# Optimization experiments

Measured on AMD Instinct MI355X. Metric: run time of the kernel, lower is better.

The kernel has to match this reference:

```python
import jax, jax.numpy as jnp
import numpy as np

WAY, NQ, C, FS = 5, 4096, 64, 5
T = FS * FS            # 25 spatial tokens
EMB = T + 1            # feature_size**2 + feature_proj_dim = 26
HEADS = 2
HD = EMB // HEADS      # 13
SCALE = HD ** -0.5
T_ATTN = 5.0           # args.temperature_attn
TEMP = 0.2             # args.temperature
LN_EPS = 1e-6


def _ln(x, g, b):
    m = x.mean(-1, keepdims=True)
    v = jnp.mean((x - m) ** 2, axis=-1, keepdims=True)
    return (x - m) / jnp.sqrt(v + LN_EPS) * g + b


def _block(x, p):
    # pre-LN transformer block (timm-style), x: (B, T, EMB)
    h = _ln(x, p['ln1_g'], p['ln1_b'])
    qkv = h @ p['qkv_w'].T + p['qkv_b']                       # (B,T,3*EMB)
    B, N, _ = qkv.shape
    qkv = qkv.reshape(B, N, 3, HEADS, HD).transpose(2, 0, 3, 1, 4)
    q, k, v = qkv[0], qkv[1], qkv[2]                          # (B,H,T,hd)
    a = jax.nn.softmax(jnp.einsum('bhqd,bhkd->bhqk', q, k) * SCALE, axis=-1)
    o = jnp.einsum('bhqk,bhkd->bhqd', a, v).transpose(0, 2, 1, 3).reshape(B, N, EMB)
    x = x + o @ p['attn_w'].T + p['attn_b']
    h = _ln(x, p['ln2_g'], p['ln2_b'])
    h = jax.nn.gelu(h @ p['fc1_w'].T + p['fc1_b'], approximate=False)
    return x + h @ p['fc2_w'].T + p['fc2_b']


def _decoder(corr, src, tgt, p):
    # CATs TransformerAggregator, num_hyperpixel=1, depth=1
    # corr: (B,1,T,T); src/tgt: (B,1,T,1) projected features
    pos = jnp.concatenate([
        jnp.broadcast_to(p['pos_x'], (1, 1, FS, FS, EMB // 2)),
        jnp.broadcast_to(p['pos_y'], (1, 1, FS, FS, EMB // 2))], axis=-1).reshape(1, 1, T, EMB)
    B = corr.shape[0]
    x = jnp.concatenate([jnp.swapaxes(corr, -1, -2), tgt], axis=3) + pos
    x = _block(x.reshape(B, T, EMB), p)
    x = (x @ p['dec_w'].T + p['dec_b']).reshape(B, 1, T, T)
    x = jnp.swapaxes(x, -1, -2) + corr            # swap axes for second self-attn pass
    x = jnp.concatenate([x, src], axis=3) + pos
    x = _block(x.reshape(B, T, EMB), p)           # same block weights reused
    x = (x @ p['dec_w'].T + p['dec_b']).reshape(B, 1, T, T) + corr
    return x.mean(axis=1)                         # (B,T,T)


def _forward(spt, qry, proj_w, proj_b, pos_x, pos_y, ln1_g, ln1_b, qkv_w, qkv_b,
             attn_w, attn_b, ln2_g, ln2_b, fc1_w, fc1_b, fc2_w, fc2_b, dec_w, dec_b):
    p = dict(pos_x=pos_x, pos_y=pos_y, ln1_g=ln1_g, ln1_b=ln1_b, qkv_w=qkv_w,
             qkv_b=qkv_b, attn_w=attn_w, attn_b=attn_b, ln2_g=ln2_g, ln2_b=ln2_b,
             fc1_w=fc1_w, fc1_b=fc1_b, fc2_w=fc2_w, fc2_b=fc2_b, dec_w=dec_w, dec_b=dec_b)
    # normalize_feature: subtract channel mean
    spt = spt - spt.mean(axis=1, keepdims=True)
    qry = qry - qry.mean(axis=1, keepdims=True)
    spt_f = jnp.broadcast_to(spt[None], (NQ, WAY, C, FS, FS)).reshape(-1, C, FS, FS)
    qry_f = jnp.broadcast_to(qry[:, None], (NQ, WAY, C, FS, FS)).reshape(-1, C, FS, FS)

    def l2n(x):  # FeatureL2Norm over channel dim
        return x / jnp.sqrt(jnp.sum(x * x, axis=1, keepdims=True) + 1e-6)

    s = l2n(spt_f).reshape(-1, C, T)
    t = l2n(qry_f).reshape(-1, C, T)
    corr = jnp.einsum('bci,bcj->bij', s, t)[:, None]                  # (B,1,T,T)
    sp = (jnp.swapaxes(spt_f.reshape(-1, C, T), 1, 2) @ proj_w.T + proj_b)[:, None]
    tp = (jnp.swapaxes(qry_f.reshape(-1, C, T), 1, 2) @ proj_w.T + proj_b)[:, None]
    refined = _decoder(corr, sp, tp, p)                               # (B,T,T)

    corr_s = refined.reshape(NQ, WAY, T, FS, FS)
    corr_q = refined.reshape(NQ, WAY, FS, FS, T)

    def gnorm(x, axis):  # torch.var is unbiased (ddof=1)
        m = x.mean(axis=axis, keepdims=True)
        v = jnp.var(x, axis=axis, keepdims=True, ddof=1)
        return (x - m) / jnp.sqrt(v + 1e-5)

    corr_s = jax.nn.softmax(gnorm(corr_s, 2) / T_ATTN, axis=2).reshape(NQ, WAY, FS, FS, FS, FS)
    corr_q = jax.nn.softmax(gnorm(corr_q, 4) / T_ATTN, axis=4).reshape(NQ, WAY, FS, FS, FS, FS)
    attn_s = corr_s.sum(axis=(4, 5))                                  # (NQ,WAY,FS,FS)
    attn_q = corr_q.sum(axis=(2, 3))
    spt_att = attn_s[:, :, None] * spt[None]                          # (NQ,WAY,C,FS,FS)
    qry_att = attn_q[:, :, None] * qry[:, None]
    sp_p = spt_att.mean(axis=(-1, -2))                                # (NQ,WAY,C)
    qp_p = qry_att.mean(axis=(-1, -2))
    n1 = jnp.maximum(jnp.linalg.norm(sp_p, axis=-1), 1e-8)
    n2 = jnp.maximum(jnp.linalg.norm(qp_p, axis=-1), 1e-8)
    sim = jnp.sum(sp_p * qp_p, axis=-1) / (n1 * n2)                   # (NQ,WAY)
    return sim / TEMP


def setup_inputs() -> dict:
    key = jax.random.key(0)
    ks = jax.random.split(key, 12)

    def w(i, shape, s=0.02):
        return jax.random.normal(ks[i], shape, jnp.float32) * s

    return {
        'spt': jax.random.normal(ks[0], (WAY, C, FS, FS), jnp.float32),
        'qry': jax.random.normal(ks[1], (NQ, C, FS, FS), jnp.float32),
        'proj_w': w(2, (1, C)), 'proj_b': jnp.zeros((1,), jnp.float32),
        'pos_x': w(3, (1, 1, 1, FS, EMB // 2)),
        'pos_y': w(4, (1, 1, FS, 1, EMB // 2)),
        'ln1_g': jnp.ones((EMB,), jnp.float32), 'ln1_b': jnp.zeros((EMB,), jnp.float32),
        'qkv_w': w(5, (3 * EMB, EMB)), 'qkv_b': jnp.zeros((3 * EMB,), jnp.float32),
        'attn_w': w(6, (EMB, EMB)), 'attn_b': jnp.zeros((EMB,), jnp.float32),
        'ln2_g': jnp.ones((EMB,), jnp.float32), 'ln2_b': jnp.zeros((EMB,), jnp.float32),
        'fc1_w': w(7, (4 * EMB, EMB)), 'fc1_b': jnp.zeros((4 * EMB,), jnp.float32),
        'fc2_w': w(8, (EMB, 4 * EMB)), 'fc2_b': jnp.zeros((EMB,), jnp.float32),
        'dec_w': w(9, (T, EMB)), 'dec_b': jnp.zeros((T,), jnp.float32),
    }


def reference(spt, qry, proj_w, proj_b, pos_x, pos_y, ln1_g, ln1_b, qkv_w, qkv_b,
              attn_w, attn_b, ln2_g, ln2_b, fc1_w, fc1_b, fc2_w, fc2_b, dec_w, dec_b):
    return _forward(spt, qry, proj_w, proj_b, pos_x, pos_y, ln1_g, ln1_b, qkv_w, qkv_b,
                    attn_w, attn_b, ln2_g, ln2_b, fc1_w, fc1_b, fc2_w, fc2_b, dec_w, dec_b)
```

## Files before the change

### kernel.cpp

```cpp
#include <hip/hip_runtime.h>
#include <math.h>

#define WAYS 5
#define NQN 4096
#define NBATCH (NQN*WAYS)

#define WS_SC 0
#define WS_RS 8000
#define WS_SP 8125
#define WS_QM 8250
#define WS_QR 110650
#define WS_TP 213050

#define WSYNC() do { asm volatile("s_waitcnt lgkmcnt(0)" ::: "memory"); __builtin_amdgcn_wave_barrier(); } while(0)

__global__ void prep_spt(const float* __restrict__ spt, const float* __restrict__ proj_w,
                         const float* __restrict__ proj_b, float* __restrict__ ws) {
    int tid = threadIdx.x;
    if (tid >= 125) return;
    int w = tid / 25, i = tid % 25;
    const float* base = spt + w * 1600 + i;
    float s = 0.f;
    for (int c = 0; c < 64; c++) s += base[c * 25];
    float m = s * (1.f / 64.f);
    float ss = 0.f, pj = 0.f;
    for (int c = 0; c < 64; c++) {
        float v = base[c * 25] - m;
        ss += v * v; pj += v * proj_w[c];
    }
    float rinv = rsqrtf(ss + 1e-6f);
    for (int c = 0; c < 64; c++)
        ws[WS_SC + (w * 25 + i) * 64 + c] = (base[c * 25] - m) * rinv;
    ws[WS_RS + w * 25 + i] = rinv;
    ws[WS_SP + w * 25 + i] = pj + proj_b[0];
}

__global__ void prep_qry(const float* __restrict__ qry, const float* __restrict__ proj_w,
                         const float* __restrict__ proj_b, float* __restrict__ ws) {
    int idx = blockIdx.x * 256 + threadIdx.x;
    if (idx >= NQN * 25) return;
    int q = idx / 25, j = idx % 25;
    const float* base = qry + q * 1600 + j;
    float s = 0.f;
    for (int c = 0; c < 64; c++) s += base[c * 25];
    float m = s * (1.f / 64.f);
    float ss = 0.f, pj = 0.f;
    for (int c = 0; c < 64; c++) {
        float v = base[c * 25] - m;
        ss += v * v; pj += v * proj_w[c];
    }
    ws[WS_QM + idx] = m;
    ws[WS_QR + idx] = rsqrtf(ss + 1e-6f);
    ws[WS_TP + idx] = pj + proj_b[0];
}

template<int M, int N, int K, int TM, int TN, int SA, int WN, int SO, int VW,
         bool ADD, bool GELU>
__device__ __forceinline__ void mmw(const float* __restrict__ A, const float* __restrict__ W,
                                    const float* __restrict__ bias, float* __restrict__ O,
                                    int lane) {
    static_assert(M % TM == 0 && N % TN == 0, "tile");
    static_assert(K % VW == 0, "vec");
    constexpr int GM = M / TM, GN = N / TN, ITEMS = GM * GN;
    constexpr int FULL = (ITEMS / 64) * 64;
    constexpr int REMO = (ITEMS - FULL) * TM * TN;
    constexpr bool SCT = (ITEMS > FULL) && (REMO <= 64);
    constexpr int LIM = SCT ? FULL : ITEMS;

    for (int v = lane; v < LIM; v += 64) {
        const int m0 = (v / GN) * TM, n0 = (v % GN) * TN;
        float acc[TM][TN];
#pragma unroll
        for (int a = 0; a < TM; a++)
#pragma unroll
            for (int c = 0; c < TN; c++) acc[a][c] = 0.f;

        if constexpr (VW == 4) {
#pragma unroll
            for (int k = 0; k < K; k += 4) {
                float4 av[TM], wv[TN];
#pragma unroll
                for (int a = 0; a < TM; a++) av[a] = *(const float4*)(A + (m0 + a) * SA + k);
#pragma unroll
                for (int c = 0; c < TN; c++) wv[c] = *(const float4*)(W + (n0 + c) * WN + k);
#pragma unroll
                for (int a = 0; a < TM; a++)
#pragma unroll
                    for (int c = 0; c < TN; c++) {
                        acc[a][c] += av[a].x * wv[c].x;
                        acc[a][c] += av[a].y * wv[c].y;
                        acc[a][c] += av[a].z * wv[c].z;
                        acc[a][c] += av[a].w * wv[c].w;
                    }
            }
        } else {
#pragma unroll 4
            for (int k = 0; k < K; k += 2) {
                float2 av[TM], wv[TN];
#pragma unroll
                for (int a = 0; a < TM; a++) av[a] = *(const float2*)(A + (m0 + a) * SA + k);
#pragma unroll
                for (int c = 0; c < TN; c++) wv[c] = *(const float2*)(W + (n0 + c) * WN + k);
#pragma unroll
                for (int a = 0; a < TM; a++)
#pragma unroll
                    for (int c = 0; c < TN; c++) {
                        acc[a][c] += av[a].x * wv[c].x;
                        acc[a][c] += av[a].y * wv[c].y;
                    }
            }
        }
#pragma unroll
        for (int a = 0; a < TM; a++)
#pragma unroll
            for (int c = 0; c < TN; c++) {
                int n = n0 + c;
                float r = acc[a][c] + (bias ? bias[n] : 0.f);
                if (GELU) r = 0.5f * r * (1.f + erff(r * 0.70710678118654752f));
                if (ADD) O[(m0 + a) * SO + n] += r; else O[(m0 + a) * SO + n] = r;
            }
    }
    if constexpr (SCT) {
        if (lane < REMO) {
            const int t = FULL + lane / (TM * TN), r0 = lane % (TM * TN);
            const int m = (t / GN) * TM + r0 / TN, n = (t % GN) * TN + r0 % TN;
            float acc = 0.f;
#pragma unroll 4
            for (int k = 0; k < K; k += 2) {
                float2 a2 = *(const float2*)(A + m * SA + k);
                float2 w2 = *(const float2*)(W + n * WN + k);
                acc += a2.x * w2.x;
                acc += a2.y * w2.y;
            }
            float r = acc + (bias ? bias[n] : 0.f);
            if (GELU) r = 0.5f * r * (1.f + erff(r * 0.70710678118654752f));
            if (ADD) O[m * SO + n] += r; else O[m * SO + n] = r;
        }
    }
}

__device__ __forceinline__ void ln_row(const float* __restrict__ x, float* __restrict__ h,
                                       const float* __restrict__ g, const float* __restrict__ bb) {
    float s = 0.f;
#pragma unroll
    for (int e = 0; e < 26; e++) s += x[e];
    float m = s * (1.f / 26.f);
    float vv = 0.f;
#pragma unroll
    for (int e = 0; e < 26; e++) { float d = x[e] - m; vv += d * d; }
    float r = rsqrtf(vv * (1.f / 26.f) + 1e-6f);
#pragma unroll
    for (int e = 0; e < 26; e++) h[e] = (x[e] - m) * r * g[e] + bb[e];
}

__global__ void __launch_bounds__(256, 2)
fused_kernel(const float* __restrict__ qry, const float* __restrict__ ws,
             const float* __restrict__ pos_x, const float* __restrict__ pos_y,
             const float* __restrict__ qkv_w, const float* __restrict__ qkv_b,
             const float* __restrict__ attn_w, const float* __restrict__ attn_b,
             const float* __restrict__ ln1_g, const float* __restrict__ ln1_b,
             const float* __restrict__ ln2_g, const float* __restrict__ ln2_b,
             const float* __restrict__ fc1_w, const float* __restrict__ fc1_b,
             const float* __restrict__ fc2_w, const float* __restrict__ fc2_b,
             const float* __restrict__ dec_w, const float* __restrict__ dec_b,
             float* __restrict__ out) {
    __shared__ __align__(16) float lds[4][4096];
    const int wid = threadIdx.x >> 6, lane = threadIdx.x & 63;
    const int b = blockIdx.x * 4 + wid, q = b / WAYS, w = b % WAYS;

    float* xm    = lds[wid];
    float* hm    = xm + 650;
    float* corrm = xm + 1300;
    float* sm    = xm + 1925;
    float* scr   = xm + 1992;

    if (lane < 25) {
        sm[lane]      = ws[WS_QM + q * 25 + lane];
        sm[32 + lane] = ws[WS_QR + q * 25 + lane];
    }
    WSYNC();

    for (int e = lane; e < 1600; e += 64) {
        int c = e / 25, j = e - c * 25;
        scr[j * 68 + c] = (qry[q * 1600 + e] - sm[j]) * sm[32 + j];
    }
    WSYNC();

    mmw<25, 25, 64, 5, 1, 64, 68, 25, 4, false, false>(ws + WS_SC + w * 1600, scr, nullptr, corrm, lane);
    WSYNC();

    for (int e = lane; e < 650; e += 64) {
        int t = e / 26, d = e - t * 26;
        float p = (d < 13) ? pos_x[(t % 5) * 13 + d] : pos_y[(t / 5) * 13 + (d - 13)];
        float base = (d < 25) ? corrm[d * 25 + t] : ws[WS_TP + q * 25 + t];
        xm[e] = base + p;
    }
    WSYNC();

    for (int it = 0; it < 2; ++it) {
        if (lane < 25) ln_row(xm + lane * 26, hm + lane * 26, ln1_g, ln1_b);
        WSYNC();
        mmw<25, 26, 26, 5, 2, 26, 26, 84, 2, false, false>(hm, qkv_w,        qkv_b,      scr,      lane);
        mmw<25, 26, 26, 5, 2, 26, 26, 84, 2, false, false>(hm, qkv_w + 676,  qkv_b + 26, scr + 28, lane);
        mmw<25, 26, 26, 5, 2, 26, 26, 84, 2, false, false>(hm, qkv_w + 1352, qkv_b + 52, scr + 56, lane);
        WSYNC();
        if (lane < 50) {
            int h = lane / 25, i = lane - h * 25;
            const float* qb = scr + i * 84 + h * 13;
            float qv[13];
#pragma unroll
            for (int k = 0; k < 13; k++) qv[k] = qb[k];
            float P[25];
            float mx = -1e30f;
#pragma unroll
            for (int j = 0; j < 25; j++) {
                const float* kb = scr + j * 84 + 28 + h * 13;
                float a = 0.f;
#pragma unroll
                for (int k = 0; k < 13; k++) a += qv[k] * kb[k];
                a *= 0.27735009811261457f;
                P[j] = a; mx = fmaxf(mx, a);
            }
            float s = 0.f;
#pragma unroll
            for (int j = 0; j < 25; j++) { P[j] = __expf(P[j] - mx); s += P[j]; }
            float inv = 1.f / s;
            float o[13];
#pragma unroll
            for (int n = 0; n < 13; n++) o[n] = 0.f;
#pragma unroll
            for (int k = 0; k < 25; k++) {
                const float* vb = scr + k * 84 + 56 + h * 13;
                float p = P[k];
#pragma unroll
                for (int n = 0; n < 13; n++) o[n] += p * vb[n];
            }
            float* ob = hm + i * 26 + h * 13;
#pragma unroll
            for (int n = 0; n < 13; n++) ob[n] = o[n] * inv;
        }
        WSYNC();
        mmw<25, 26, 26, 5, 2, 26, 26, 26, 2, true, false>(hm, attn_w, attn_b, xm, lane);
        WSYNC();
        if (lane < 25) ln_row(xm + lane * 26, hm + lane * 26, ln2_g, ln2_b);
        WSYNC();
        mmw<25, 52, 26, 5, 4, 26, 26, 52, 2, false, true>(hm, fc1_w, fc1_b, scr, lane);
        WSYNC();
        mmw<25, 26, 52, 5, 2, 52, 104, 26, 2, true, false>(scr, fc2_w, fc2_b, xm, lane);
        WSYNC();
        mmw<25, 52, 26, 5, 4, 26, 26, 52, 2, false, true>(hm, fc1_w + 1352, fc1_b + 52, scr, lane);
        WSYNC();
        mmw<25, 26, 52, 5, 2, 52, 104, 26, 2, true, false>(scr, fc2_w + 52, nullptr, xm, lane);
        WSYNC();
        mmw<25, 25, 26, 5, 1, 26, 26, 25, 2, false, false>(xm, dec_w, dec_b, scr, lane);
        WSYNC();
        if (it == 0) {
            for (int e = lane; e < 650; e += 64) {
                int t = e / 26, d = e - t * 26;
                float p = (d < 13) ? pos_x[(t % 5) * 13 + d] : pos_y[(t / 5) * 13 + (d - 13)];
                float base = (d < 25) ? (scr[d * 25 + t] + corrm[t * 25 + d]) : ws[WS_SP + w * 25 + t];
                xm[e] = base + p;
            }
            WSYNC();
        }
    }

    for (int e = lane; e < 625; e += 64) scr[e] += corrm[e];
    WSYNC();

    if (lane < 25) {
        int j = lane;
        float s = 0.f;
        for (int i = 0; i < 25; i++) s += scr[i * 25 + j];
        float m = s * 0.04f;
        float ss = 0.f;
        for (int i = 0; i < 25; i++) { float d = scr[i * 25 + j] - m; ss += d * d; }
        float rinv = rsqrtf(ss * (1.f / 24.f) + 1e-5f) * 0.2f;
        float mx = -1e30f;
        for (int i = 0; i < 25; i++) { float z = (scr[i * 25 + j] - m) * rinv; corrm[i * 25 + j] = z; mx = fmaxf(mx, z); }
        float se = 0.f;
        for (int i = 0; i < 25; i++) { float e2 = __expf(corrm[i * 25 + j] - mx); corrm[i * 25 + j] = e2; se += e2; }
        float inv = 1.f / se;
        for (int i = 0; i < 25; i++) corrm[i * 25 + j] *= inv;
    }
    WSYNC();
    if (lane < 25) {
        int i = lane; float s = 0.f;
        for (int j = 0; j < 25; j++) s += corrm[i * 25 + j];
        hm[i] = s * 0.04f / ws[WS_RS + w * 25 + i];
    }
    WSYNC();
    if (lane < 25) {
        int i = lane;
        float s = 0.f;
        for (int j = 0; j < 25; j++) s += scr[i * 25 + j];
        float m = s * 0.04f;
        float ss = 0.f;
        for (int j = 0; j < 25; j++) { float d = scr[i * 25 + j] - m; ss += d * d; }
        float rinv = rsqrtf(ss * (1.f / 24.f) + 1e-5f) * 0.2f;
        float mx = -1e30f;
        for (int j = 0; j < 25; j++) { float z = (scr[i * 25 + j] - m) * rinv; corrm[i * 25 + j] = z; mx = fmaxf(mx, z); }
        float se = 0.f;
        for (int j = 0; j < 25; j++) { float e2 = __expf(corrm[i * 25 + j] - mx); corrm[i * 25 + j] = e2; se += e2; }
        float inv = 1.f / se;
        for (int j = 0; j < 25; j++) corrm[i * 25 + j] *= inv;
    }
    WSYNC();
    if (lane < 25) {
        int j = lane; float s = 0.f;
        for (int i = 0; i < 25; i++) s += corrm[i * 25 + j];
        hm[32 + j] = s * 0.04f / sm[32 + j];
    }
    WSYNC();

    for (int e = lane; e < 1600; e += 64) {
        int c = e / 25, j = e - c * 25;
        scr[e] = (qry[q * 1600 + e] - sm[j]) * sm[32 + j];
    }
    WSYNC();

    {
        float sv = 0.f, qv2 = 0.f;
        const float* snb = ws + WS_SC + w * 1600 + lane;
        for (int i = 0; i < 25; i++) sv  += hm[i]      * snb[i * 64];
        for (int j = 0; j < 25; j++) qv2 += hm[32 + j] * scr[lane * 25 + j];
        float d = sv * qv2, n1 = sv * sv, n2 = qv2 * qv2;
#pragma unroll
        for (int msk = 32; msk >= 1; msk >>= 1) {
            d  += __shfl_xor(d,  msk);
            n1 += __shfl_xor(n1, msk);
            n2 += __shfl_xor(n2, msk);
        }
        if (lane == 0) {
            n1 = fmaxf(sqrtf(n1), 1e-8f);
            n2 = fmaxf(sqrtf(n2), 1e-8f);
            out[b] = d / (n1 * n2) * 5.f;
        }
    }
}

extern "C" void kernel_launch(void* const* d_in, const int* in_sizes, int n_in,
                              void* d_out, int out_size, void* d_ws, size_t ws_size,
                              hipStream_t stream) {
    const float* spt    = (const float*)d_in[0];
    const float* qry    = (const float*)d_in[1];
    const float* proj_w = (const float*)d_in[2];
    const float* proj_b = (const float*)d_in[3];
    const float* pos_x  = (const float*)d_in[4];
    const float* pos_y  = (const float*)d_in[5];
    const float* ln1_g  = (const float*)d_in[6];
    const float* ln1_b  = (const float*)d_in[7];
    const float* qkv_w  = (const float*)d_in[8];
    const float* qkv_b  = (const float*)d_in[9];
    const float* attn_w = (const float*)d_in[10];
    const float* attn_b = (const float*)d_in[11];
    const float* ln2_g  = (const float*)d_in[12];
    const float* ln2_b  = (const float*)d_in[13];
    const float* fc1_w  = (const float*)d_in[14];
    const float* fc1_b  = (const float*)d_in[15];
    const float* fc2_w  = (const float*)d_in[16];
    const float* fc2_b  = (const float*)d_in[17];
    const float* dec_w  = (const float*)d_in[18];
    const float* dec_b  = (const float*)d_in[19];
    float* ws  = (float*)d_ws;
    float* out = (float*)d_out;

    prep_spt<<<1, 128, 0, stream>>>(spt, proj_w, proj_b, ws);
    prep_qry<<<(NQN * 25 + 255) / 256, 256, 0, stream>>>(qry, proj_w, proj_b, ws);
    fused_kernel<<<NBATCH / 4, 256, 0, stream>>>(qry, ws, pos_x, pos_y, qkv_w, qkv_b, attn_w, attn_b,
                                                 ln1_g, ln1_b, ln2_g, ln2_b, fc1_w, fc1_b,
                                                 fc2_w, fc2_b, dec_w, dec_b, out);
}
```

Baseline: 1.302 ms.

## Process each batch item with two waves instead of one in fused kernel

Each batch item is now handled by 128 threads (two wavefronts) instead of one wavefront, so a 256-thread block covers two items instead of four and the grid doubles. The matmul helper gains a thread-count parameter, the three QKV matmuls are merged into one 78-wide GEMM, the two attention heads and the row/column softmax passes are split across the two waves, and the final cosine reduction is split between waves. This shortens the serial per-item critical path and raises launch bounds to four blocks per CU. In exchange, cheap wave-level syncs become block-wide __syncthreads, and many phases leave the second wave idle.

Result: slower. 1.544 ms (+18.6%).

```diff
diff --git a/kernel.cpp b/kernel.cpp
--- a/kernel.cpp
+++ b/kernel.cpp
@@ -11,8 +11,6 @@
 #define WS_QM 8250
 #define WS_QR 110650
 #define WS_TP 213050
-
-#define WSYNC() do { asm volatile("s_waitcnt lgkmcnt(0)" ::: "memory"); __builtin_amdgcn_wave_barrier(); } while(0)
 
 __global__ void prep_spt(const float* __restrict__ spt, const float* __restrict__ proj_w,
                          const float* __restrict__ proj_b, float* __restrict__ ws) {
@@ -55,19 +53,19 @@
 }
 
 template<int M, int N, int K, int TM, int TN, int SA, int WN, int SO, int VW,
-         bool ADD, bool GELU>
+         bool ADD, bool GELU, int TC>
 __device__ __forceinline__ void mmw(const float* __restrict__ A, const float* __restrict__ W,
                                     const float* __restrict__ bias, float* __restrict__ O,
-                                    int lane) {
+                                    int tid) {
     static_assert(M % TM == 0 && N % TN == 0, "tile");
     static_assert(K % VW == 0, "vec");
     constexpr int GM = M / TM, GN = N / TN, ITEMS = GM * GN;
-    constexpr int FULL = (ITEMS / 64) * 64;
+    constexpr int FULL = (ITEMS / TC) * TC;
     constexpr int REMO = (ITEMS - FULL) * TM * TN;
-    constexpr bool SCT = (ITEMS > FULL) && (REMO <= 64);
+    constexpr bool SCT = (ITEMS > FULL) && (FULL > 0) && (REMO <= TC);
     constexpr int LIM = SCT ? FULL : ITEMS;
 
-    for (int v = lane; v < LIM; v += 64) {
+    for (int v = tid; v < LIM; v += TC) {
         const int m0 = (v / GN) * TM, n0 = (v % GN) * TN;
         float acc[TM][TN];
 #pragma unroll
@@ -121,8 +119,8 @@
             }
     }
     if constexpr (SCT) {
-        if (lane < REMO) {
-            const int t = FULL + lane / (TM * TN), r0 = lane % (TM * TN);
+        if (tid < REMO) {
+            const int t = FULL + tid / (TM * TN), r0 = tid % (TM * TN);
             const int m = (t / GN) * TM + r0 / TN, n = (t % GN) * TN + r0 % TN;
             float acc = 0.f;
 #pragma unroll 4
@@ -153,7 +151,7 @@
     for (int e = 0; e < 26; e++) h[e] = (x[e] - m) * r * g[e] + bb[e];
 }
 
-__global__ void __launch_bounds__(256, 2)
+__global__ void __launch_bounds__(256, 4)
 fused_kernel(const float* __restrict__ qry, const float* __restrict__ ws,
              const float* __restrict__ pos_x, const float* __restrict__ pos_y,
              const float* __restrict__ qkv_w, const float* __restrict__ qkv_b,
@@ -164,49 +162,49 @@
              const float* __restrict__ fc2_w, const float* __restrict__ fc2_b,
              const float* __restrict__ dec_w, const float* __restrict__ dec_b,
              float* __restrict__ out) {
-    __shared__ __align__(16) float lds[4][4096];
-    const int wid = threadIdx.x >> 6, lane = threadIdx.x & 63;
-    const int b = blockIdx.x * 4 + wid, q = b / WAYS, w = b % WAYS;
-
-    float* xm    = lds[wid];
+    __shared__ __align__(16) float lds[2][4096];
+    const int half = threadIdx.x >> 7;
+    const int tid  = threadIdx.x & 127;
+    const int w2   = tid >> 6, lane = tid & 63;
+    const int b = blockIdx.x * 2 + half, q = b / WAYS, w = b % WAYS;
+
+    float* xm    = lds[half];
     float* hm    = xm + 650;
     float* corrm = xm + 1300;
     float* sm    = xm + 1925;
     float* scr   = xm + 1992;
 
-    if (lane < 25) {
-        sm[lane]      = ws[WS_QM + q * 25 + lane];
-        sm[32 + lane] = ws[WS_QR + q * 25 + lane];
-    }
-    WSYNC();
-
-    for (int e = lane; e < 1600; e += 64) {
+    if (tid < 25) {
+        sm[tid]      = ws[WS_QM + q * 25 + tid];
+        sm[32 + tid] = ws[WS_QR + q * 25 + tid];
+    }
+    __syncthreads();
+
+    for (int e = tid; e < 1600; e += 128) {
         int c = e / 25, j = e - c * 25;
         scr[j * 68 + c] = (qry[q * 1600 + e] - sm[j]) * sm[32 + j];
     }
-    WSYNC();
-
-    mmw<25, 25, 64, 5, 1, 64, 68, 25, 4, false, false>(ws + WS_SC + w * 1600, scr, nullptr, corrm, lane);
-    WSYNC();
-
-    for (int e = lane; e < 650; e += 64) {
+    __syncthreads();
+
+    mmw<25, 25, 64, 5, 1, 64, 68, 25, 4, false, false, 128>(ws + WS_SC + w * 1600, scr, nullptr, corrm, tid);
+    __syncthreads();
+
+    for (int e = tid; e < 650; e += 128) {
         int t = e / 26, d = e - t * 26;
         float p = (d < 13) ? pos_x[(t % 5) * 13 + d] : pos_y[(t / 5) * 13 + (d - 13)];
         float base = (d < 25) ? corrm[d * 25 + t] : ws[WS_TP + q * 25 + t];
         xm[e] = base + p;
     }
-    WSYNC();
+    __syncthreads();
 
     for (int it = 0; it < 2; ++it) {
-        if (lane < 25) ln_row(xm + lane * 26, hm + lane * 26, ln1_g, ln1_b);
-        WSYNC();
-        mmw<25, 26, 26, 5, 2, 26, 26, 84, 2, false, false>(hm, qkv_w,        qkv_b,      scr,      lane);
-        mmw<25, 26, 26, 5, 2, 26, 26, 84, 2, false, false>(hm, qkv_w + 676,  qkv_b + 26, scr + 28, lane);
-        mmw<25, 26, 26, 5, 2, 26, 26, 84, 2, false, false>(hm, qkv_w + 1352, qkv_b + 52, scr + 56, lane);
-        WSYNC();
-        if (lane < 50) {
-            int h = lane / 25, i = lane - h * 25;
-            const float* qb = scr + i * 84 + h * 13;
+        { int r = w2 * 13 + lane; if (lane < 13 - w2) ln_row(xm + r * 26, hm + r * 26, ln1_g, ln1_b); }
+        __syncthreads();
+        mmw<25, 78, 26, 5, 3, 26, 26, 78, 2, false, false, 128>(hm, qkv_w, qkv_b, scr, tid);
+        __syncthreads();
+        if (lane < 25) {
+            const int h = w2, i = lane;
+            const float* qb = scr + i * 78 + h * 13;
             float qv[13];
 #pragma unroll
             for (int k = 0; k < 13; k++) qv[k] = qb[k];
@@ -214,7 +212,7 @@
             float mx = -1e30f;
 #pragma unroll
             for (int j = 0; j < 25; j++) {
-                const float* kb = scr + j * 84 + 28 + h * 13;
+                const float* kb = scr + j * 78 + 26 + h * 13;
                 float a = 0.f;
 #pragma unroll
                 for (int k = 0; k < 13; k++) a += qv[k] * kb[k];
@@ -230,7 +228,7 @@
             for (int n = 0; n < 13; n++) o[n] = 0.f;
 #pragma unroll
             for (int k = 0; k < 25; k++) {
-                const float* vb = scr + k * 84 + 56 + h * 13;
+                const float* vb = scr + k * 78 + 52 + h * 13;
                 float p = P[k];
 #pragma unroll
                 for (int n = 0; n < 13; n++) o[n] += p * vb[n];
@@ -239,92 +237,100 @@
 #pragma unroll
             for (int n = 0; n < 13; n++) ob[n] = o[n] * inv;
         }
-        WSYNC();
-        mmw<25, 26, 26, 5, 2, 26, 26, 26, 2, true, false>(hm, attn_w, attn_b, xm, lane);
-        WSYNC();
-        if (lane < 25) ln_row(xm + lane * 26, hm + lane * 26, ln2_g, ln2_b);
-        WSYNC();
-        mmw<25, 52, 26, 5, 4, 26, 26, 52, 2, false, true>(hm, fc1_w, fc1_b, scr, lane);
-        WSYNC();
-        mmw<25, 26, 52, 5, 2, 52, 104, 26, 2, true, false>(scr, fc2_w, fc2_b, xm, lane);
-        WSYNC();
-        mmw<25, 52, 26, 5, 4, 26, 26, 52, 2, false, true>(hm, fc1_w + 1352, fc1_b + 52, scr, lane);
-        WSYNC();
-        mmw<25, 26, 52, 5, 2, 52, 104, 26, 2, true, false>(scr, fc2_w + 52, nullptr, xm, lane);
-        WSYNC();
-        mmw<25, 25, 26, 5, 1, 26, 26, 25, 2, false, false>(xm, dec_w, dec_b, scr, lane);
-        WSYNC();
+        __syncthreads();
+        mmw<25, 26, 26, 5, 1, 26, 26, 26, 2, true, false, 128>(hm, attn_w, attn_b, xm, tid);
+        __syncthreads();
+        { int r = w2 * 13 + lane; if (lane < 13 - w2) ln_row(xm + r * 26, hm + r * 26, ln2_g, ln2_b); }
+        __syncthreads();
+        mmw<25, 52, 26, 5, 2, 26, 26, 52, 2, false, true, 128>(hm, fc1_w, fc1_b, scr, tid);
+        __syncthreads();
+        mmw<25, 26, 52, 5, 1, 52, 104, 26, 2, true, false, 128>(scr, fc2_w, fc2_b, xm, tid);
+        __syncthreads();
+        mmw<25, 52, 26, 5, 2, 26, 26, 52, 2, false, true, 128>(hm, fc1_w + 1352, fc1_b + 52, scr, tid);
+        __syncthreads();
+        mmw<25, 26, 52, 5, 1, 52, 104, 26, 2, true, false, 128>(scr, fc2_w + 52, nullptr, xm, tid);
+        __syncthreads();
+        mmw<25, 25, 26, 5, 1, 26, 26, 25, 2, false, false, 128>(xm, dec_w, dec_b, scr, tid);
+        __syncthreads();
         if (it == 0) {
-            for (int e = lane; e < 650; e += 64) {
+            for (int e = tid; e < 650; e += 128) {
                 int t = e / 26, d = e - t * 26;
                 float p = (d < 13) ? pos_x[(t % 5) * 13 + d] : pos_y[(t / 5) * 13 + (d - 13)];
                 float base = (d < 25) ? (scr[d * 25 + t] + corrm[t * 25 + d]) : ws[WS_SP + w * 25 + t];
                 xm[e] = base + p;
             }
-            WSYNC();
-        }
-    }
-
-    for (int e = lane; e < 625; e += 64) scr[e] += corrm[e];
-    WSYNC();
+            __syncthreads();
+        }
+    }
+
+    for (int e = tid; e < 625; e += 128) scr[e] += corrm[e];
+    __syncthreads();
 
     if (lane < 25) {
-        int j = lane;
-        float s = 0.f;
-        for (int i = 0; i < 25; i++) s += scr[i * 25 + j];
-        float m = s * 0.04f;
-        float ss = 0.f;
-        for (int i = 0; i < 25; i++) { float d = scr[i * 25 + j] - m; ss += d * d; }
-        float rinv = rsqrtf(ss * (1.f / 24.f) + 1e-5f) * 0.2f;
-        float mx = -1e30f;
-        for (int i = 0; i < 25; i++) { float z = (scr[i * 25 + j] - m) * rinv; corrm[i * 25 + j] = z; mx = fmaxf(mx, z); }
-        float se = 0.f;
-        for (int i = 0; i < 25; i++) { float e2 = __expf(corrm[i * 25 + j] - mx); corrm[i * 25 + j] = e2; se += e2; }
-        float inv = 1.f / se;
-        for (int i = 0; i < 25; i++) corrm[i * 25 + j] *= inv;
-    }
-    WSYNC();
+        if (w2 == 0) {
+            int j = lane;
+            float s = 0.f;
+            for (int i = 0; i < 25; i++) s += scr[i * 25 + j];
+            float m = s * 0.04f;
+            float ss = 0.f;
+            for (int i = 0; i < 25; i++) { float d = scr[i * 25 + j] - m; ss += d * d; }
+            float rinv = rsqrtf(ss * (1.f / 24.f) + 1e-5f) * 0.2f;
+            float mx = -1e30f;
+            for (int i = 0; i < 25; i++) { float z = (scr[i * 25 + j] - m) * rinv; corrm[i * 25 + j] = z; mx = fmaxf(mx, z); }
+            float se = 0.f;
+            for (int i = 0; i < 25; i++) { float e2 = __expf(corrm[i * 25 + j] - mx); corrm[i * 25 + j] = e2; se += e2; }
+            float inv = 1.f / se;
+            for (int i = 0; i < 25; i++) corrm[i * 25 + j] *= inv;
+        } else {
+            int i = lane;
+            float s = 0.f;
+            for (int j = 0; j < 25; j++) s += scr[i * 25 + j];
+            float m = s * 0.04f;
+            float ss = 0.f;
+            for (int j = 0; j < 25; j++) { float d = scr[i * 25 + j] - m; ss += d * d; }
+            float rinv = rsqrtf(ss * (1.f / 24.f) + 1e-5f) * 0.2f;
+            float mx = -1e30f;
+            for (int j = 0; j < 25; j++) { float z = (scr[i * 25 + j] - m) * rinv; xm[i * 25 + j] = z; mx = fmaxf(mx, z); }
+            float se = 0.f;
+            for (int j = 0; j < 25; j++) { float e2 = __expf(xm[i * 25 + j] - mx); xm[i * 25 + j] = e2; se += e2; }
+            float inv = 1.f / se;
+            for (int j = 0; j < 25; j++) xm[i * 25 + j] *= inv;
+        }
+    }
+    __syncthreads();
     if (lane < 25) {
-        int i = lane; float s = 0.f;
-        for (int j = 0; j < 25; j++) s += corrm[i * 25 + j];
-        hm[i] = s * 0.04f / ws[WS_RS + w * 25 + i];
-    }
-    WSYNC();
-    if (lane < 25) {
-        int i = lane;
-        float s = 0.f;
-        for (int j = 0; j < 25; j++) s += scr[i * 25 + j];
-        float m = s * 0.04f;
-        float ss = 0.f;
-        for (int j = 0; j < 25; j++) { float d = scr[i * 25 + j] - m; ss += d * d; }
-        float rinv = rsqrtf(ss * (1.f / 24.f) + 1e-5f) * 0.2f;
-        float mx = -1e30f;
-        for (int j = 0; j < 25; j++) { float z = (scr[i * 25 + j] - m) * rinv; corrm[i * 25 + j] = z; mx = fmaxf(mx, z); }
-        float se = 0.f;
-        for (int j = 0; j < 25; j++) { float e2 = __expf(corrm[i * 25 + j] - mx); corrm[i * 25 + j] = e2; se += e2; }
-        float inv = 1.f / se;
-        for (int j = 0; j < 25; j++) corrm[i * 25 + j] *= inv;
-    }
-    WSYNC();
-    if (lane < 25) {
-        int j = lane; float s = 0.f;
-        for (int i = 0; i < 25; i++) s += corrm[i * 25 + j];
-        hm[32 + j] = s * 0.04f / sm[32 + j];
-    }
-    WSYNC();
-
-    for (int e = lane; e < 1600; e += 64) {
+        if (w2 == 0) {
+            int i = lane; float s = 0.f;
+            for (int j = 0; j < 25; j++) s += corrm[i * 25 + j];
+            hm[i] = s * 0.04f / ws[WS_RS + w * 25 + i];
+        } else {
+            int j = lane; float s = 0.f;
+            for (int i = 0; i < 25; i++) s += xm[i * 25 + j];
+            hm[32 + j] = s * 0.04f / sm[32 + j];
+        }
+    }
+    __syncthreads();
+
+    for (int e = tid; e < 1600; e += 128) {
         int c = e / 25, j = e - c * 25;
         scr[e] = (qry[q * 1600 + e] - sm[j]) * sm[32 + j];
     }
-    WSYNC();
-
-    {
-        float sv = 0.f, qv2 = 0.f;
+    __syncthreads();
+
+    if (w2 == 0) {
+        float sv = 0.f;
         const float* snb = ws + WS_SC + w * 1600 + lane;
-        for (int i = 0; i < 25; i++) sv  += hm[i]      * snb[i * 64];
+        for (int i = 0; i < 25; i++) sv += hm[i] * snb[i * 64];
+        corrm[lane] = sv;
+    } else {
+        float qv2 = 0.f;
         for (int j = 0; j < 25; j++) qv2 += hm[32 + j] * scr[lane * 25 + j];
-        float d = sv * qv2, n1 = sv * sv, n2 = qv2 * qv2;
+        corrm[64 + lane] = qv2;
+    }
+    __syncthreads();
+    if (w2 == 0) {
+        float a = corrm[lane], b2 = corrm[64 + lane];
+        float d = a * b2, n1 = a * a, n2 = b2 * b2;
 #pragma unroll
         for (int msk = 32; msk >= 1; msk >>= 1) {
             d  += __shfl_xor(d,  msk);
@@ -367,7 +373,7 @@
 
     prep_spt<<<1, 128, 0, stream>>>(spt, proj_w, proj_b, ws);
     prep_qry<<<(NQN * 25 + 255) / 256, 256, 0, stream>>>(qry, proj_w, proj_b, ws);
-    fused_kernel<<<NBATCH / 4, 256, 0, stream>>>(qry, ws, pos_x, pos_y, qkv_w, qkv_b, attn_w, attn_b,
+    fused_kernel<<<NBATCH / 2, 256, 0, stream>>>(qry, ws, pos_x, pos_y, qkv_w, qkv_b, attn_w, attn_b,
                                                  ln1_g, ln1_b, ln2_g, ln2_b, fc1_w, fc1_b,
                                                  fc2_w, fc2_b, dec_w, dec_b, out);
 }
```

## Shrink per-wave LDS footprint by precomputing normalized queries and recomputing correlation

Applied to the files above, without the earlier changes.

prep_qry now writes the normalized query features in token-major order to the workspace. The fused kernel reads them straight from global memory for the correlation GEMM instead of staging them in LDS, and it recomputes the correlation matrix rather than keeping a persistent corr buffer. QKV is computed one projection at a time and the MLP is split into four 26-wide chunks, so the scratch buffers shrink and LDS per wave drops from 4096 to 1952 floats, which allows more blocks per CU. The cost is extra global reads, extra GEMM work, more wave barriers, and more live registers (qv, P) carried across phases.

New measurement: 1.663 ms. 27.8% more time.

```diff
diff --git a/kernel.cpp b/kernel.cpp
--- a/kernel.cpp
+++ b/kernel.cpp
@@ -8,9 +8,9 @@
 #define WS_SC 0
 #define WS_RS 8000
 #define WS_SP 8125
-#define WS_QM 8250
-#define WS_QR 110650
-#define WS_TP 213050
+#define WS_QR 8250
+#define WS_TP 110650
+#define WS_QN 213052
 
 #define WSYNC() do { asm volatile("s_waitcnt lgkmcnt(0)" ::: "memory"); __builtin_amdgcn_wave_barrier(); } while(0)
 
@@ -49,25 +49,27 @@
         float v = base[c * 25] - m;
         ss += v * v; pj += v * proj_w[c];
     }
-    ws[WS_QM + idx] = m;
-    ws[WS_QR + idx] = rsqrtf(ss + 1e-6f);
+    float rinv = rsqrtf(ss + 1e-6f);
+    float* qn = ws + WS_QN + q * 1600 + j * 64;
+    for (int c = 0; c < 64; c++) qn[c] = (base[c * 25] - m) * rinv;
+    ws[WS_QR + idx] = rinv;
     ws[WS_TP + idx] = pj + proj_b[0];
 }
 
 template<int M, int N, int K, int TM, int TN, int SA, int WN, int SO, int VW,
-         bool ADD, bool GELU>
+         bool ADD, bool GELU, int TC>
 __device__ __forceinline__ void mmw(const float* __restrict__ A, const float* __restrict__ W,
                                     const float* __restrict__ bias, float* __restrict__ O,
-                                    int lane) {
+                                    int tid) {
     static_assert(M % TM == 0 && N % TN == 0, "tile");
     static_assert(K % VW == 0, "vec");
     constexpr int GM = M / TM, GN = N / TN, ITEMS = GM * GN;
-    constexpr int FULL = (ITEMS / 64) * 64;
+    constexpr int FULL = (ITEMS / TC) * TC;
     constexpr int REMO = (ITEMS - FULL) * TM * TN;
-    constexpr bool SCT = (ITEMS > FULL) && (REMO <= 64);
+    constexpr bool SCT = (ITEMS > FULL) && (FULL > 0) && (REMO <= TC);
     constexpr int LIM = SCT ? FULL : ITEMS;
 
-    for (int v = lane; v < LIM; v += 64) {
+    for (int v = tid; v < LIM; v += TC) {
         const int m0 = (v / GN) * TM, n0 = (v % GN) * TN;
         float acc[TM][TN];
 #pragma unroll
@@ -121,8 +123,8 @@
             }
     }
     if constexpr (SCT) {
-        if (lane < REMO) {
-            const int t = FULL + lane / (TM * TN), r0 = lane % (TM * TN);
+        if (tid < REMO) {
+            const int t = FULL + tid / (TM * TN), r0 = tid % (TM * TN);
             const int m = (t / GN) * TM + r0 / TN, n = (t % GN) * TN + r0 % TN;
             float acc = 0.f;
 #pragma unroll 4
@@ -164,35 +166,26 @@
              const float* __restrict__ fc2_w, const float* __restrict__ fc2_b,
              const float* __restrict__ dec_w, const float* __restrict__ dec_b,
              float* __restrict__ out) {
-    __shared__ __align__(16) float lds[4][4096];
+    __shared__ __align__(16) float lds[4 * 1952];
     const int wid = threadIdx.x >> 6, lane = threadIdx.x & 63;
     const int b = blockIdx.x * 4 + wid, q = b / WAYS, w = b % WAYS;
 
-    float* xm    = lds[wid];
-    float* hm    = xm + 650;
-    float* corrm = xm + 1300;
-    float* sm    = xm + 1925;
-    float* scr   = xm + 1992;
-
-    if (lane < 25) {
-        sm[lane]      = ws[WS_QM + q * 25 + lane];
-        sm[32 + lane] = ws[WS_QR + q * 25 + lane];
-    }
-    WSYNC();
-
-    for (int e = lane; e < 1600; e += 64) {
-        int c = e / 25, j = e - c * 25;
-        scr[j * 68 + c] = (qry[q * 1600 + e] - sm[j]) * sm[32 + j];
-    }
-    WSYNC();
-
-    mmw<25, 25, 64, 5, 1, 64, 68, 25, 4, false, false>(ws + WS_SC + w * 1600, scr, nullptr, corrm, lane);
+    float* xm  = lds + wid * 1952;
+    float* hm  = xm + 650;
+    float* scr = xm + 1300;
+
+    const float* scg = ws + WS_SC + w * 1600;
+    const float* qng = ws + WS_QN + q * 1600;
+
+    const int h = lane / 25, ii = lane - h * 25;
+
+    mmw<25, 25, 64, 5, 1, 64, 64, 25, 4, false, false, 64>(scg, qng, nullptr, scr, lane);
     WSYNC();
 
     for (int e = lane; e < 650; e += 64) {
         int t = e / 26, d = e - t * 26;
         float p = (d < 13) ? pos_x[(t % 5) * 13 + d] : pos_y[(t / 5) * 13 + (d - 13)];
-        float base = (d < 25) ? corrm[d * 25 + t] : ws[WS_TP + q * 25 + t];
+        float base = (d < 25) ? scr[d * 25 + t] : ws[WS_TP + q * 25 + t];
         xm[e] = base + p;
     }
     WSYNC();
@@ -200,21 +193,22 @@
     for (int it = 0; it < 2; ++it) {
         if (lane < 25) ln_row(xm + lane * 26, hm + lane * 26, ln1_g, ln1_b);
         WSYNC();
-        mmw<25, 26, 26, 5, 2, 26, 26, 84, 2, false, false>(hm, qkv_w,        qkv_b,      scr,      lane);
-        mmw<25, 26, 26, 5, 2, 26, 26, 84, 2, false, false>(hm, qkv_w + 676,  qkv_b + 26, scr + 28, lane);
-        mmw<25, 26, 26, 5, 2, 26, 26, 84, 2, false, false>(hm, qkv_w + 1352, qkv_b + 52, scr + 56, lane);
+        float qv[13], P[25], inv;
+        mmw<25, 26, 26, 5, 2, 26, 26, 26, 2, false, false, 64>(hm, qkv_w, qkv_b, scr, lane);
         WSYNC();
         if (lane < 50) {
-            int h = lane / 25, i = lane - h * 25;
-            const float* qb = scr + i * 84 + h * 13;
-            float qv[13];
+            const float* qb = scr + ii * 26 + h * 13;
 #pragma unroll
             for (int k = 0; k < 13; k++) qv[k] = qb[k];
-            float P[25];
+        }
+        WSYNC();
+        mmw<25, 26, 26, 5, 2, 26, 26, 26, 2, false, false, 64>(hm, qkv_w + 676, qkv_b + 26, scr, lane);
+        WSYNC();
+        if (lane < 50) {
             float mx = -1e30f;
 #pragma unroll
             for (int j = 0; j < 25; j++) {
-                const float* kb = scr + j * 84 + 28 + h * 13;
+                const float* kb = scr + j * 26 + h * 13;
                 float a = 0.f;
 #pragma unroll
                 for (int k = 0; k < 13; k++) a += qv[k] * kb[k];
@@ -224,48 +218,56 @@
             float s = 0.f;
 #pragma unroll
             for (int j = 0; j < 25; j++) { P[j] = __expf(P[j] - mx); s += P[j]; }
-            float inv = 1.f / s;
+            inv = 1.f / s;
+        }
+        WSYNC();
+        mmw<25, 26, 26, 5, 2, 26, 26, 26, 2, false, false, 64>(hm, qkv_w + 1352, qkv_b + 52, scr, lane);
+        WSYNC();
+        if (lane < 50) {
             float o[13];
 #pragma unroll
             for (int n = 0; n < 13; n++) o[n] = 0.f;
 #pragma unroll
             for (int k = 0; k < 25; k++) {
-                const float* vb = scr + k * 84 + 56 + h * 13;
+                const float* vb = scr + k * 26 + h * 13;
                 float p = P[k];
 #pragma unroll
                 for (int n = 0; n < 13; n++) o[n] += p * vb[n];
             }
-            float* ob = hm + i * 26 + h * 13;
+            float* ob = hm + ii * 26 + h * 13;
 #pragma unroll
             for (int n = 0; n < 13; n++) ob[n] = o[n] * inv;
         }
         WSYNC();
-        mmw<25, 26, 26, 5, 2, 26, 26, 26, 2, true, false>(hm, attn_w, attn_b, xm, lane);
+        mmw<25, 26, 26, 5, 2, 26, 26, 26, 2, true, false, 64>(hm, attn_w, attn_b, xm, lane);
         WSYNC();
         if (lane < 25) ln_row(xm + lane * 26, hm + lane * 26, ln2_g, ln2_b);
         WSYNC();
-        mmw<25, 52, 26, 5, 4, 26, 26, 52, 2, false, true>(hm, fc1_w, fc1_b, scr, lane);
-        WSYNC();
-        mmw<25, 26, 52, 5, 2, 52, 104, 26, 2, true, false>(scr, fc2_w, fc2_b, xm, lane);
-        WSYNC();
-        mmw<25, 52, 26, 5, 4, 26, 26, 52, 2, false, true>(hm, fc1_w + 1352, fc1_b + 52, scr, lane);
-        WSYNC();
-        mmw<25, 26, 52, 5, 2, 52, 104, 26, 2, true, false>(scr, fc2_w + 52, nullptr, xm, lane);
-        WSYNC();
-        mmw<25, 25, 26, 5, 1, 26, 26, 25, 2, false, false>(xm, dec_w, dec_b, scr, lane);
+#pragma unroll
+        for (int Qt = 0; Qt < 4; ++Qt) {
+            mmw<25, 26, 26, 5, 2, 26, 26, 26, 2, false, true, 64>(hm, fc1_w + 676 * Qt,
+                                                                  fc1_b + 26 * Qt, scr, lane);
+            WSYNC();
+            mmw<25, 26, 26, 5, 2, 26, 104, 26, 2, true, false, 64>(scr, fc2_w + 26 * Qt,
+                                                                   Qt == 0 ? fc2_b : nullptr, xm, lane);
+            WSYNC();
+        }
+        mmw<25, 25, 26, 5, 1, 26, 26, 25, 2, false, false, 64>(xm, dec_w, dec_b, scr, lane);
         WSYNC();
         if (it == 0) {
+            mmw<25, 25, 64, 5, 1, 64, 64, 25, 4, true, false, 64>(qng, scg, nullptr, scr, lane);
+            WSYNC();
             for (int e = lane; e < 650; e += 64) {
                 int t = e / 26, d = e - t * 26;
                 float p = (d < 13) ? pos_x[(t % 5) * 13 + d] : pos_y[(t / 5) * 13 + (d - 13)];
-                float base = (d < 25) ? (scr[d * 25 + t] + corrm[t * 25 + d]) : ws[WS_SP + w * 25 + t];
+                float base = (d < 25) ? scr[d * 25 + t] : ws[WS_SP + w * 25 + t];
                 xm[e] = base + p;
             }
             WSYNC();
         }
     }
 
-    for (int e = lane; e < 625; e += 64) scr[e] += corrm[e];
+    mmw<25, 25, 64, 5, 1, 64, 64, 25, 4, true, false, 64>(scg, qng, nullptr, scr, lane);
     WSYNC();
 
     if (lane < 25) {
@@ -277,19 +279,12 @@
         for (int i = 0; i < 25; i++) { float d = scr[i * 25 + j] - m; ss += d * d; }
         float rinv = rsqrtf(ss * (1.f / 24.f) + 1e-5f) * 0.2f;
         float mx = -1e30f;
-        for (int i = 0; i < 25; i++) { float z = (scr[i * 25 + j] - m) * rinv; corrm[i * 25 + j] = z; mx = fmaxf(mx, z); }
+        for (int i = 0; i < 25; i++) { float z = (scr[i * 25 + j] - m) * rinv; xm[i * 25 + j] = z; mx = fmaxf(mx, z); }
         float se = 0.f;
-        for (int i = 0; i < 25; i++) { float e2 = __expf(corrm[i * 25 + j] - mx); corrm[i * 25 + j] = e2; se += e2; }
-        float inv = 1.f / se;
-        for (int i = 0; i < 25; i++) corrm[i * 25 + j] *= inv;
-    }
-    WSYNC();
-    if (lane < 25) {
-        int i = lane; float s = 0.f;
-        for (int j = 0; j < 25; j++) s += corrm[i * 25 + j];
-        hm[i] = s * 0.04f / ws[WS_RS + w * 25 + i];
-    }
-    WSYNC();
+        for (int i = 0; i < 25; i++) { float e2 = __expf(xm[i * 25 + j] - mx); xm[i * 25 + j] = e2; se += e2; }
+        float iv = 1.f / se;
+        for (int i = 0; i < 25; i++) xm[i * 25 + j] *= iv;
+    }
     if (lane < 25) {
         int i = lane;
         float s = 0.f;
@@ -299,31 +294,31 @@
         for (int j = 0; j < 25; j++) { float d = scr[i * 25 + j] - m; ss += d * d; }
         float rinv = rsqrtf(ss * (1.f / 24.f) + 1e-5f) * 0.2f;
         float mx = -1e30f;
-        for (int j = 0; j < 25; j++) { float z = (scr[i * 25 + j] - m) * rinv; corrm[i * 25 + j] = z; mx = fmaxf(mx, z); }
+        for (int j = 0; j < 25; j++) { float z = (scr[i * 25 + j] - m) * rinv; hm[i * 25 + j] = z; mx = fmaxf(mx, z); }
         float se = 0.f;
-        for (int j = 0; j < 25; j++) { float e2 = __expf(corrm[i * 25 + j] - mx); corrm[i * 25 + j] = e2; se += e2; }
-        float inv = 1.f / se;
-        for (int j = 0; j < 25; j++) corrm[i * 25 + j] *= inv;
-    }
-    WSYNC();
+        for (int j = 0; j < 25; j++) { float e2 = __expf(hm[i * 25 + j] - mx); hm[i * 25 + j] = e2; se += e2; }
+        float iv = 1.f / se;
+        for (int j = 0; j < 25; j++) hm[i * 25 + j] *= iv;
+    }
+    WSYNC();
+    if (lane < 25) {
+        int i = lane; float s = 0.f;
+        for (int j = 0; j < 25; j++) s += xm[i * 25 + j];
+        scr[i] = s * 0.04f / ws[WS_RS + w * 25 + i];
+    }
     if (lane < 25) {
         int j = lane; float s = 0.f;
-        for (int i = 0; i < 25; i++) s += corrm[i * 25 + j];
-        hm[32 + j] = s * 0.04f / sm[32 + j];
-    }
-    WSYNC();
-
-    for (int e = lane; e < 1600; e += 64) {
-        int c = e / 25, j = e - c * 25;
-        scr[e] = (qry[q * 1600 + e] - sm[j]) * sm[32 + j];
+        for (int i = 0; i < 25; i++) s += hm[i * 25 + j];
+        scr[32 + j] = s * 0.04f / ws[WS_QR + q * 25 + j];
     }
     WSYNC();
 
     {
         float sv = 0.f, qv2 = 0.f;
-        const float* snb = ws + WS_SC + w * 1600 + lane;
-        for (int i = 0; i < 25; i++) sv  += hm[i]      * snb[i * 64];
-        for (int j = 0; j < 25; j++) qv2 += hm[32 + j] * scr[lane * 25 + j];
+        const float* snb = scg + lane;
+        for (int i = 0; i < 25; i++) sv += scr[i] * snb[i * 64];
+        const float* qnb = qng + lane;
+        for (int j = 0; j < 25; j++) qv2 += scr[32 + j] * qnb[j * 64];
         float d = sv * qv2, n1 = sv * sv, n2 = qv2 * qv2;
 #pragma unroll
         for (int msk = 32; msk >= 1; msk >>= 1) {
```
